# Kernel optimization log

Hardware: AMD Instinct MI355X
Metric: run time of the kernel (lower is better)

Reference implementation:

```python
import jax, jax.numpy as jnp
import numpy as np

NEG_INF = -9.0e15  # matches torch's -9000000000000000.0 mask value
ALPHA = 0.2        # LeakyReLU negative slope from init_kwargs


def setup_inputs() -> dict:
    key = jax.random.key(0)
    k1, k2, k3, k4, k5 = jax.random.split(key, 5)
    B, N, D, A = 64, 128, 128, 1000
    hidden = jax.random.normal(k1, (B, N, D), dtype=jnp.float32)
    adj = jax.random.randint(k2, (B, N, N), 0, 5)  # edge types 0..4 (0 = masked)
    a = jax.random.normal(k3, (D, 4), dtype=jnp.float32) * 0.1  # stacked a_0..a_3
    A_attr_sess = jax.random.uniform(k4, (B, N, A), dtype=jnp.float32)
    attr_embedding = jax.random.normal(k5, (A, D), dtype=jnp.float32)
    return {"hidden": hidden, "adj": adj, "a": a,
            "A_attr_sess": A_attr_sess, "attr_embedding": attr_embedding}


def reference(hidden, adj, a, A_attr_sess, attr_embedding):
    # a_input[b,i,j,:] = leaky_relu(h[b,i,:] * h[b,j,:])  -> [B,N,N,D]
    a_input = jax.nn.leaky_relu(hidden[:, :, None, :] * hidden[:, None, :, :],
                                negative_slope=ALPHA)
    # four edge-type scores in one contraction: [B,N,N,4]
    e = jnp.einsum('bijd,dk->bijk', a_input, a)
    # masked selection by adjacency edge type (later writes override earlier)
    alpha = jnp.full(adj.shape, NEG_INF, dtype=e.dtype)
    alpha = jnp.where(adj == 1, e[..., 0], alpha)
    alpha = jnp.where(adj == 2, e[..., 1], alpha)
    alpha = jnp.where(adj == 3, e[..., 2], alpha)
    alpha = jnp.where(adj == 4, e[..., 3], alpha)
    attn = jax.nn.softmax(alpha, axis=-1)        # [B,N,N]
    output = jnp.einsum('bij,bjd->bid', attn, hidden)  # [B,N,D]
    attr_sess = jnp.einsum('bna,ad->bnd', A_attr_sess, attr_embedding)
    return output, attr_sess
```

## Files before the change

### kernel.cpp

```cpp
#include <hip/hip_runtime.h>

#define BB 64
#define NN 128
#define DD 128
#define AA 1000
#define KPAD 1024
#define NEG_INF (-9.0e15f)

typedef __attribute__((ext_vector_type(8))) short short8;
typedef __attribute__((ext_vector_type(4))) float floatx4;
typedef __attribute__((ext_vector_type(4))) unsigned int uintx4;
typedef __attribute__((ext_vector_type(2))) unsigned int uintx2;

__device__ __forceinline__ float bflo(unsigned int u) { return __uint_as_float(u << 16); }
__device__ __forceinline__ float bfhi(unsigned int u) { return __uint_as_float(u & 0xffff0000u); }
__device__ __forceinline__ unsigned int packbf(float f0, float f1) {
  return (__float_as_uint(f0) >> 16) | (__float_as_uint(f1) & 0xffff0000u);
}
__device__ __forceinline__ unsigned short bf_rne(float f) {
  unsigned int u = __float_as_uint(f);
  return (unsigned short)((u + 0x7fffu + ((u >> 16) & 1u)) >> 16);
}
__device__ __forceinline__ unsigned int packbf_rne(float f0, float f1) {
  return (unsigned int)bf_rne(f0) | ((unsigned int)bf_rne(f1) << 16);
}
__device__ __forceinline__ short8 u2s(uintx4 v) {
  union { uintx4 u; short8 s; } x; x.u = v; return x.s;
}

__global__ __launch_bounds__(256) void prep_kernel(
    const float* __restrict__ hidden, const float* __restrict__ emb,
    unsigned short* __restrict__ ET, unsigned short* __restrict__ Hbf,
    unsigned short* __restrict__ HTg)
{
  const int t = threadIdx.x;
  const int bid = blockIdx.x;
  if (bid < BB) {
    __shared__ float hsf[NN * 129];
    const float* hb = hidden + (size_t)bid * NN * DD;
    #pragma unroll
    for (int u = 0; u < 16; ++u) {
      int e = u * 1024 + t * 4;
      float4 v = *reinterpret_cast<const float4*>(hb + e);
      int r = e >> 7, c = e & 127;
      float* d = &hsf[r * 129 + c];
      d[0] = v.x; d[1] = v.y; d[2] = v.z; d[3] = v.w;
    }
    __syncthreads();
    unsigned short* hb16 = Hbf + (size_t)bid * NN * DD;
    unsigned short* ht16 = HTg + (size_t)bid * NN * DD;
    #pragma unroll
    for (int u = 0; u < 8; ++u) {
      int e = u * 2048 + t * 8;
      int r = e >> 7, c = e & 127;
      const float* src = &hsf[r * 129 + c];
      uintx4 o;
      o.x = packbf_rne(src[0], src[1]); o.y = packbf_rne(src[2], src[3]);
      o.z = packbf_rne(src[4], src[5]); o.w = packbf_rne(src[6], src[7]);
      *reinterpret_cast<uintx4*>(hb16 + e) = o;
    }
    #pragma unroll
    for (int u = 0; u < 8; ++u) {
      int e = u * 2048 + t * 8;
      int dI = e >> 7, il = e & 127;
      float x[8];
      #pragma unroll
      for (int j = 0; j < 8; ++j) x[j] = hsf[(il + j) * 129 + dI];
      uintx4 o;
      o.x = packbf_rne(x[0], x[1]); o.y = packbf_rne(x[2], x[3]);
      o.z = packbf_rne(x[4], x[5]); o.w = packbf_rne(x[6], x[7]);
      *reinterpret_cast<uintx4*>(ht16 + e) = o;
    }
  } else {
    int c = bid - BB;
    int k0 = t * 4;
    float x[4];
    #pragma unroll
    for (int j = 0; j < 4; ++j) {
      int k = k0 + j;
      x[j] = (k < AA) ? emb[(size_t)k * DD + c] : 0.f;
    }
    uintx2 o;
    o.x = packbf_rne(x[0], x[1]);
    o.y = packbf_rne(x[2], x[3]);
    *reinterpret_cast<uintx2*>(ET + (size_t)c * KPAD + k0) = o;
  }
}

struct AttnSmem {
  __align__(16) unsigned short Hs[NN * 128];
  __align__(16) unsigned short As[4 * 16 * 256];
  __align__(16) float Sa[16 * 129];
  union {
    __align__(16) float saf[4 * 256];
    __align__(16) unsigned short W[16 * 128];
  } u;
};

__global__ __launch_bounds__(256, 2) void attn_kernel(
    const int* __restrict__ adj, const float* __restrict__ amat,
    const unsigned short* __restrict__ Hbf,
    const unsigned short* __restrict__ HTg,
    float* __restrict__ out0)
{
  __shared__ AttnSmem s;
  const int t = threadIdx.x;
  const int L = t & 63, w = t >> 6;
  const int lr = L & 15, lq = L >> 4;
  const int b = blockIdx.x >> 3;
  const int i0 = (blockIdx.x & 7) * 16;

  const unsigned short* hb = Hbf + (size_t)b * NN * DD;
  #pragma unroll
  for (int u = 0; u < 8; ++u) {
    int id = u * 256 + t;
    int r = id >> 4, c = id & 15;
    uintx4 v = *reinterpret_cast<const uintx4*>(hb + r * 128 + c * 8);
    *reinterpret_cast<uintx4*>(&s.Hs[r * 128 + ((c ^ (r & 15)) << 3)]) = v;
  }
  {
    float v1 = amat[t], v2 = amat[t + 256];
    int dI = t >> 2, k = t & 3;
    s.u.saf[k * 256 + dI] = 0.6f * v1;
    s.u.saf[k * 256 + 128 + dI] = 0.4f * v1;
    s.u.saf[k * 256 + 64 + dI] = 0.6f * v2;
    s.u.saf[k * 256 + 192 + dI] = 0.4f * v2;
  }
  __syncthreads();

  #pragma unroll
  for (int u = 0; u < 8; ++u) {
    int id = u * 256 + t;
    int k = id >> 9, ii = (id >> 5) & 15, c = id & 31;
    int srow = i0 + ii;
    int dchunk = c & 15;
    uintx4 hv = *reinterpret_cast<const uintx4*>(
        &s.Hs[srow * 128 + ((dchunk ^ (srow & 15)) << 3)]);
    if (c & 16) {
      hv.x &= 0x7fff7fffu; hv.y &= 0x7fff7fffu;
      hv.z &= 0x7fff7fffu; hv.w &= 0x7fff7fffu;
    }
    const float* sf = &s.u.saf[k * 256 + c * 8];
    uintx4 o;
    o.x = packbf(bflo(hv.x) * sf[0], bfhi(hv.x) * sf[1]);
    o.y = packbf(bflo(hv.y) * sf[2], bfhi(hv.y) * sf[3]);
    o.z = packbf(bflo(hv.z) * sf[4], bfhi(hv.z) * sf[5]);
    o.w = packbf(bflo(hv.w) * sf[6], bfhi(hv.w) * sf[7]);
    *reinterpret_cast<uintx4*>(&s.As[k * 4096 + ii * 256 + ((c ^ ii) << 3)]) = o;
  }
  __syncthreads();

  floatx4 acc[4][2];
  #pragma unroll
  for (int k = 0; k < 4; ++k)
    #pragma unroll
    for (int nt = 0; nt < 2; ++nt) acc[k][nt] = floatx4{0.f, 0.f, 0.f, 0.f};

  #pragma unroll
  for (int kt = 0; kt < 8; ++kt) {
    int ca = lq + 4 * kt;
    short8 afr[4];
    #pragma unroll
    for (int k = 0; k < 4; ++k)
      afr[k] = *reinterpret_cast<const short8*>(
          &s.As[k * 4096 + lr * 256 + ((ca ^ lr) << 3)]);
    int cb = lq + 4 * (kt & 3);
    short8 bfr[2];
    #pragma unroll
    for (int nt = 0; nt < 2; ++nt) {
      int jrow = w * 32 + nt * 16 + lr;
      uintx4 hv = *reinterpret_cast<const uintx4*>(
          &s.Hs[jrow * 128 + ((cb ^ (jrow & 15)) << 3)]);
      if (kt >= 4) {
        hv.x &= 0x7fff7fffu; hv.y &= 0x7fff7fffu;
        hv.z &= 0x7fff7fffu; hv.w &= 0x7fff7fffu;
      }
      bfr[nt] = u2s(hv);
    }
    #pragma unroll
    for (int k = 0; k < 4; ++k)
      #pragma unroll
      for (int nt = 0; nt < 2; ++nt)
        acc[k][nt] = __builtin_amdgcn_mfma_f32_16x16x32_bf16(
            afr[k], bfr[nt], acc[k][nt], 0, 0, 0);
  }

  short8 pvb[2][4];
  const unsigned short* ht = HTg + (size_t)b * NN * DD;
  #pragma unroll
  for (int nt = 0; nt < 2; ++nt)
    #pragma unroll
    for (int kt = 0; kt < 4; ++kt) {
      int dI = w * 32 + nt * 16 + lr;
      pvb[nt][kt] = *reinterpret_cast<const short8*>(ht + dI * 128 + kt * 32 + lq * 8);
    }

  const int* adjb = adj + ((size_t)b * NN + i0) * NN;
  #pragma unroll
  for (int nt = 0; nt < 2; ++nt)
    #pragma unroll
    for (int r = 0; r < 4; ++r) {
      int ii = lq * 4 + r;
      int j = w * 32 + nt * 16 + lr;
      int ad = adjb[ii * NN + j];
      float al = NEG_INF;
      al = (ad == 1) ? acc[0][nt][r] : al;
      al = (ad == 2) ? acc[1][nt][r] : al;
      al = (ad == 3) ? acc[2][nt][r] : al;
      al = (ad == 4) ? acc[3][nt][r] : al;
      s.Sa[ii * 129 + j] = al;
    }
  __syncthreads();

  #pragma unroll
  for (int p = 0; p < 4; ++p) {
    int ii = w * 4 + p;
    float a1 = s.Sa[ii * 129 + L];
    float a2 = s.Sa[ii * 129 + 64 + L];
    float m = fmaxf(a1, a2);
    #pragma unroll
    for (int off = 32; off > 0; off >>= 1) m = fmaxf(m, __shfl_xor(m, off, 64));
    float e1 = __expf(fmaxf(a1 - m, -80.f));
    float e2 = __expf(fmaxf(a2 - m, -80.f));
    float ss = e1 + e2;
    #pragma unroll
    for (int off = 32; off > 0; off >>= 1) ss += __shfl_xor(ss, off, 64);
    float inv = 1.f / ss;
    int j2 = L + 64;
    s.u.W[ii * 128 + (((L >> 3) ^ ii) << 3) + (L & 7)] = bf_rne(e1 * inv);
    s.u.W[ii * 128 + (((j2 >> 3) ^ ii) << 3) + (j2 & 7)] = bf_rne(e2 * inv);
  }
  __syncthreads();

  floatx4 oacc[2];
  oacc[0] = floatx4{0.f, 0.f, 0.f, 0.f};
  oacc[1] = floatx4{0.f, 0.f, 0.f, 0.f};
  #pragma unroll
  for (int kt = 0; kt < 4; ++kt) {
    int c = lq + 4 * kt;
    short8 wf = *reinterpret_cast<const short8*>(
        &s.u.W[lr * 128 + ((c ^ lr) << 3)]);
    #pragma unroll
    for (int nt = 0; nt < 2; ++nt)
      oacc[nt] = __builtin_amdgcn_mfma_f32_16x16x32_bf16(
          wf, pvb[nt][kt], oacc[nt], 0, 0, 0);
  }
  float* ob = out0 + ((size_t)b * NN + i0) * DD;
  #pragma unroll
  for (int nt = 0; nt < 2; ++nt)
    #pragma unroll
    for (int r = 0; r < 4; ++r)
      ob[(lq * 4 + r) * DD + w * 32 + nt * 16 + lr] = oacc[nt][r];
}

#define BK 64
__global__ __launch_bounds__(256) void attr_kernel(
    const float* __restrict__ Aattr, const unsigned short* __restrict__ ET,
    float* __restrict__ out1)
{
  __shared__ __align__(16) unsigned short ETs[2][DD * BK];
  __shared__ __align__(16) unsigned short As2[2][32 * BK];

  const int t = threadIdx.x;
  const int L = t & 63, w = t >> 6;
  const int lr = L & 15, lq = L >> 4;
  const int r0 = blockIdx.x * 32;

  float4 pa0, pa1;
  uintx4 pe[4];
  const int ar = t >> 3, ak = (t & 7) * 8;
  const int ec = t >> 1, ej0 = (t & 1) * 4;

  auto fetch = [&](int it) {
    int kb = it * BK;
    int k4 = kb + ak;
    float4 z = {0.f, 0.f, 0.f, 0.f};
    pa0 = (k4 < AA) ? *reinterpret_cast<const float4*>(Aattr + (size_t)(r0 + ar) * AA + k4) : z;
    pa1 = (k4 + 4 < AA) ? *reinterpret_cast<const float4*>(Aattr + (size_t)(r0 + ar) * AA + k4 + 4) : z;
    #pragma unroll
    for (int q = 0; q < 4; ++q)
      pe[q] = *reinterpret_cast<const uintx4*>(ET + (size_t)ec * KPAD + kb + (ej0 + q) * 8);
  };
  auto stage = [&](int buf) {
    uintx4 o;
    o.x = packbf(pa0.x, pa0.y); o.y = packbf(pa0.z, pa0.w);
    o.z = packbf(pa1.x, pa1.y); o.w = packbf(pa1.z, pa1.w);
    int ac = t & 7;
    *reinterpret_cast<uintx4*>(&As2[buf][ar * BK + ((ac ^ (ar & 7)) << 3)]) = o;
    #pragma unroll
    for (int q = 0; q < 4; ++q)
      *reinterpret_cast<uintx4*>(&ETs[buf][ec * BK + (((ej0 + q) ^ (ec & 7)) << 3)]) = pe[q];
  };

  floatx4 acc[2][2];
  #pragma unroll
  for (int mt = 0; mt < 2; ++mt)
    #pragma unroll
    for (int nt = 0; nt < 2; ++nt) acc[mt][nt] = floatx4{0.f, 0.f, 0.f, 0.f};

  fetch(0);
  for (int it = 0; it < 16; ++it) {
    stage(it & 1);
    __syncthreads();
    if (it < 15) fetch(it + 1);
    #pragma unroll
    for (int ks = 0; ks < 2; ++ks) {
      int c = lq + 4 * ks;
      short8 af[2], bf[2];
      #pragma unroll
      for (int mt = 0; mt < 2; ++mt) {
        int row = mt * 16 + lr;
        af[mt] = *reinterpret_cast<const short8*>(
            &As2[it & 1][row * BK + ((c ^ (row & 7)) << 3)]);
      }
      #pragma unroll
      for (int nt = 0; nt < 2; ++nt) {
        int n = w * 32 + nt * 16 + lr;
        bf[nt] = *reinterpret_cast<const short8*>(
            &ETs[it & 1][n * BK + ((c ^ (n & 7)) << 3)]);
      }
      #pragma unroll
      for (int mt = 0; mt < 2; ++mt)
        #pragma unroll
        for (int nt = 0; nt < 2; ++nt)
          acc[mt][nt] = __builtin_amdgcn_mfma_f32_16x16x32_bf16(
              af[mt], bf[nt], acc[mt][nt], 0, 0, 0);
    }
  }

  float* ob = out1 + (size_t)r0 * DD;
  #pragma unroll
  for (int mt = 0; mt < 2; ++mt)
    #pragma unroll
    for (int nt = 0; nt < 2; ++nt)
      #pragma unroll
      for (int r = 0; r < 4; ++r)
        ob[(mt * 16 + lq * 4 + r) * DD + w * 32 + nt * 16 + lr] = acc[mt][nt][r];
}

extern "C" void kernel_launch(void* const* d_in, const int* in_sizes, int n_in,
                              void* d_out, int out_size, void* d_ws, size_t ws_size,
                              hipStream_t stream) {
  const float* hidden = (const float*)d_in[0];
  const int*   adj    = (const int*)d_in[1];
  const float* amat   = (const float*)d_in[2];
  const float* Aattr  = (const float*)d_in[3];
  const float* emb    = (const float*)d_in[4];

  float* out0 = (float*)d_out;
  float* out1 = out0 + (size_t)BB * NN * DD;

  unsigned short* ET  = (unsigned short*)d_ws;
  unsigned short* Hbf = ET + (size_t)DD * KPAD;
  unsigned short* HTg = Hbf + (size_t)BB * NN * DD;

  prep_kernel<<<BB + DD, 256, 0, stream>>>(hidden, emb, ET, Hbf, HTg);
  attn_kernel<<<BB * 8, 256, 0, stream>>>(adj, amat, Hbf, HTg, out0);
  attr_kernel<<<(BB * NN) / 32, 256, 0, stream>>>(Aattr, ET, out1);
}
```

Before: 109.8 us.

## Fuse attention and attribute GEMM into one launch with shared-memory union

Merges the attention and attribute-projection kernels into a single 768-block launch that branches on block index, so the two independent workloads run concurrently and one launch is saved. The attention path now reads fp32 hidden directly and converts to bf16 on load, dropping the bf16 copy of hidden that the prep kernel used to write. Adjacency is loaded up front so its latency overlaps the MFMA work. Shared memory is reorganised as a union to reduce the footprint, and occupancy is raised to 3 blocks per CU. The cost is an extra barrier, larger fp32 loads per attention block, and mixed block types that may balance unevenly across CUs.

```diff
diff --git a/kernel.cpp b/kernel.cpp
--- a/kernel.cpp
+++ b/kernel.cpp
@@ -30,8 +30,7 @@
 
 __global__ __launch_bounds__(256) void prep_kernel(
     const float* __restrict__ hidden, const float* __restrict__ emb,
-    unsigned short* __restrict__ ET, unsigned short* __restrict__ Hbf,
-    unsigned short* __restrict__ HTg)
+    unsigned short* __restrict__ ET, unsigned short* __restrict__ HTg)
 {
   const int t = threadIdx.x;
   const int bid = blockIdx.x;
@@ -47,18 +46,7 @@
       d[0] = v.x; d[1] = v.y; d[2] = v.z; d[3] = v.w;
     }
     __syncthreads();
-    unsigned short* hb16 = Hbf + (size_t)bid * NN * DD;
     unsigned short* ht16 = HTg + (size_t)bid * NN * DD;
-    #pragma unroll
-    for (int u = 0; u < 8; ++u) {
-      int e = u * 2048 + t * 8;
-      int r = e >> 7, c = e & 127;
-      const float* src = &hsf[r * 129 + c];
-      uintx4 o;
-      o.x = packbf_rne(src[0], src[1]); o.y = packbf_rne(src[2], src[3]);
-      o.z = packbf_rne(src[4], src[5]); o.w = packbf_rne(src[6], src[7]);
-      *reinterpret_cast<uintx4*>(hb16 + e) = o;
-    }
     #pragma unroll
     for (int u = 0; u < 8; ++u) {
       int e = u * 2048 + t * 8;
@@ -89,42 +77,63 @@
 
 struct AttnSmem {
   __align__(16) unsigned short Hs[NN * 128];
-  __align__(16) unsigned short As[4 * 16 * 256];
-  __align__(16) float Sa[16 * 129];
   union {
-    __align__(16) float saf[4 * 256];
-    __align__(16) unsigned short W[16 * 128];
-  } u;
+    __align__(16) unsigned short As[4 * 16 * 256];
+    struct {
+      __align__(16) float Sa[16 * 129];
+      __align__(16) unsigned short W[16 * 128];
+    } sw;
+  } u2;
+  __align__(16) float saf[4 * 256];
 };
 
-__global__ __launch_bounds__(256, 2) void attn_kernel(
+#define BK 64
+struct AttrSmem {
+  __align__(16) unsigned short ETs[2][DD * BK];
+  __align__(16) unsigned short As2[2][32 * BK];
+};
+
+union FusedSmem { AttnSmem a; AttrSmem g; };
+
+__device__ __forceinline__ void attn_body(
+    AttnSmem& s, const float* __restrict__ hidden,
     const int* __restrict__ adj, const float* __restrict__ amat,
-    const unsigned short* __restrict__ Hbf,
-    const unsigned short* __restrict__ HTg,
-    float* __restrict__ out0)
+    const unsigned short* __restrict__ HTg, float* __restrict__ out0)
 {
-  __shared__ AttnSmem s;
   const int t = threadIdx.x;
   const int L = t & 63, w = t >> 6;
   const int lr = L & 15, lq = L >> 4;
   const int b = blockIdx.x >> 3;
   const int i0 = (blockIdx.x & 7) * 16;
 
-  const unsigned short* hb = Hbf + (size_t)b * NN * DD;
+  const int* adjb = adj + ((size_t)b * NN + i0) * NN;
+  int adjv[8];
+  #pragma unroll
+  for (int nt = 0; nt < 2; ++nt)
+    #pragma unroll
+    for (int r = 0; r < 4; ++r)
+      adjv[nt * 4 + r] = adjb[(lq * 4 + r) * NN + w * 32 + nt * 16 + lr];
+
+  const float* hb = hidden + (size_t)b * NN * DD;
   #pragma unroll
   for (int u = 0; u < 8; ++u) {
     int id = u * 256 + t;
     int r = id >> 4, c = id & 15;
-    uintx4 v = *reinterpret_cast<const uintx4*>(hb + r * 128 + c * 8);
-    *reinterpret_cast<uintx4*>(&s.Hs[r * 128 + ((c ^ (r & 15)) << 3)]) = v;
+    const float* src = hb + r * 128 + c * 8;
+    float4 v0 = *reinterpret_cast<const float4*>(src);
+    float4 v1 = *reinterpret_cast<const float4*>(src + 4);
+    uintx4 o;
+    o.x = packbf_rne(v0.x, v0.y); o.y = packbf_rne(v0.z, v0.w);
+    o.z = packbf_rne(v1.x, v1.y); o.w = packbf_rne(v1.z, v1.w);
+    *reinterpret_cast<uintx4*>(&s.Hs[r * 128 + ((c ^ (r & 15)) << 3)]) = o;
   }
   {
     float v1 = amat[t], v2 = amat[t + 256];
     int dI = t >> 2, k = t & 3;
-    s.u.saf[k * 256 + dI] = 0.6f * v1;
-    s.u.saf[k * 256 + 128 + dI] = 0.4f * v1;
-    s.u.saf[k * 256 + 64 + dI] = 0.6f * v2;
-    s.u.saf[k * 256 + 192 + dI] = 0.4f * v2;
+    s.saf[k * 256 + dI] = 0.6f * v1;
+    s.saf[k * 256 + 128 + dI] = 0.4f * v1;
+    s.saf[k * 256 + 64 + dI] = 0.6f * v2;
+    s.saf[k * 256 + 192 + dI] = 0.4f * v2;
   }
   __syncthreads();
 
@@ -140,13 +149,13 @@
       hv.x &= 0x7fff7fffu; hv.y &= 0x7fff7fffu;
       hv.z &= 0x7fff7fffu; hv.w &= 0x7fff7fffu;
     }
-    const float* sf = &s.u.saf[k * 256 + c * 8];
+    const float* sf = &s.saf[k * 256 + c * 8];
     uintx4 o;
     o.x = packbf(bflo(hv.x) * sf[0], bfhi(hv.x) * sf[1]);
     o.y = packbf(bflo(hv.y) * sf[2], bfhi(hv.y) * sf[3]);
     o.z = packbf(bflo(hv.z) * sf[4], bfhi(hv.z) * sf[5]);
     o.w = packbf(bflo(hv.w) * sf[6], bfhi(hv.w) * sf[7]);
-    *reinterpret_cast<uintx4*>(&s.As[k * 4096 + ii * 256 + ((c ^ ii) << 3)]) = o;
+    *reinterpret_cast<uintx4*>(&s.u2.As[k * 4096 + ii * 256 + ((c ^ ii) << 3)]) = o;
   }
   __syncthreads();
 
@@ -163,7 +172,7 @@
     #pragma unroll
     for (int k = 0; k < 4; ++k)
       afr[k] = *reinterpret_cast<const short8*>(
-          &s.As[k * 4096 + lr * 256 + ((ca ^ lr) << 3)]);
+          &s.u2.As[k * 4096 + lr * 256 + ((ca ^ lr) << 3)]);
     int cb = lq + 4 * (kt & 3);
     short8 bfr[2];
     #pragma unroll
@@ -184,6 +193,7 @@
         acc[k][nt] = __builtin_amdgcn_mfma_f32_16x16x32_bf16(
             afr[k], bfr[nt], acc[k][nt], 0, 0, 0);
   }
+  __syncthreads();
 
   short8 pvb[2][4];
   const unsigned short* ht = HTg + (size_t)b * NN * DD;
@@ -195,28 +205,27 @@
       pvb[nt][kt] = *reinterpret_cast<const short8*>(ht + dI * 128 + kt * 32 + lq * 8);
     }
 
-  const int* adjb = adj + ((size_t)b * NN + i0) * NN;
   #pragma unroll
   for (int nt = 0; nt < 2; ++nt)
     #pragma unroll
     for (int r = 0; r < 4; ++r) {
       int ii = lq * 4 + r;
       int j = w * 32 + nt * 16 + lr;
-      int ad = adjb[ii * NN + j];
+      int ad = adjv[nt * 4 + r];
       float al = NEG_INF;
       al = (ad == 1) ? acc[0][nt][r] : al;
       al = (ad == 2) ? acc[1][nt][r] : al;
       al = (ad == 3) ? acc[2][nt][r] : al;
       al = (ad == 4) ? acc[3][nt][r] : al;
-      s.Sa[ii * 129 + j] = al;
+      s.u2.sw.Sa[ii * 129 + j] = al;
     }
   __syncthreads();
 
   #pragma unroll
   for (int p = 0; p < 4; ++p) {
     int ii = w * 4 + p;
-    float a1 = s.Sa[ii * 129 + L];
-    float a2 = s.Sa[ii * 129 + 64 + L];
+    float a1 = s.u2.sw.Sa[ii * 129 + L];
+    float a2 = s.u2.sw.Sa[ii * 129 + 64 + L];
     float m = fmaxf(a1, a2);
     #pragma unroll
     for (int off = 32; off > 0; off >>= 1) m = fmaxf(m, __shfl_xor(m, off, 64));
@@ -227,8 +236,8 @@
     for (int off = 32; off > 0; off >>= 1) ss += __shfl_xor(ss, off, 64);
     float inv = 1.f / ss;
     int j2 = L + 64;
-    s.u.W[ii * 128 + (((L >> 3) ^ ii) << 3) + (L & 7)] = bf_rne(e1 * inv);
-    s.u.W[ii * 128 + (((j2 >> 3) ^ ii) << 3) + (j2 & 7)] = bf_rne(e2 * inv);
+    s.u2.sw.W[ii * 128 + (((L >> 3) ^ ii) << 3) + (L & 7)] = bf_rne(e1 * inv);
+    s.u2.sw.W[ii * 128 + (((j2 >> 3) ^ ii) << 3) + (j2 & 7)] = bf_rne(e2 * inv);
   }
   __syncthreads();
 
@@ -239,7 +248,7 @@
   for (int kt = 0; kt < 4; ++kt) {
     int c = lq + 4 * kt;
     short8 wf = *reinterpret_cast<const short8*>(
-        &s.u.W[lr * 128 + ((c ^ lr) << 3)]);
+        &s.u2.sw.W[lr * 128 + ((c ^ lr) << 3)]);
     #pragma unroll
     for (int nt = 0; nt < 2; ++nt)
       oacc[nt] = __builtin_amdgcn_mfma_f32_16x16x32_bf16(
@@ -253,18 +262,14 @@
       ob[(lq * 4 + r) * DD + w * 32 + nt * 16 + lr] = oacc[nt][r];
 }
 
-#define BK 64
-__global__ __launch_bounds__(256) void attr_kernel(
-    const float* __restrict__ Aattr, const unsigned short* __restrict__ ET,
-    float* __restrict__ out1)
+__device__ __forceinline__ void attr_body(
+    AttrSmem& s, const float* __restrict__ Aattr,
+    const unsigned short* __restrict__ ET, float* __restrict__ out1)
 {
-  __shared__ __align__(16) unsigned short ETs[2][DD * BK];
-  __shared__ __align__(16) unsigned short As2[2][32 * BK];
-
   const int t = threadIdx.x;
   const int L = t & 63, w = t >> 6;
   const int lr = L & 15, lq = L >> 4;
-  const int r0 = blockIdx.x * 32;
+  const int r0 = (blockIdx.x - 512) * 32;
 
   float4 pa0, pa1;
   uintx4 pe[4];
@@ -286,10 +291,10 @@
     o.x = packbf(pa0.x, pa0.y); o.y = packbf(pa0.z, pa0.w);
     o.z = packbf(pa1.x, pa1.y); o.w = packbf(pa1.z, pa1.w);
     int ac = t & 7;
-    *reinterpret_cast<uintx4*>(&As2[buf][ar * BK + ((ac ^ (ar & 7)) << 3)]) = o;
+    *reinterpret_cast<uintx4*>(&s.As2[buf][ar * BK + ((ac ^ (ar & 7)) << 3)]) = o;
     #pragma unroll
     for (int q = 0; q < 4; ++q)
-      *reinterpret_cast<uintx4*>(&ETs[buf][ec * BK + (((ej0 + q) ^ (ec & 7)) << 3)]) = pe[q];
+      *reinterpret_cast<uintx4*>(&s.ETs[buf][ec * BK + (((ej0 + q) ^ (ec & 7)) << 3)]) = pe[q];
   };
 
   floatx4 acc[2][2];
@@ -311,13 +316,13 @@
       for (int mt = 0; mt < 2; ++mt) {
         int row = mt * 16 + lr;
         af[mt] = *reinterpret_cast<const short8*>(
-            &As2[it & 1][row * BK + ((c ^ (row & 7)) << 3)]);
+            &s.As2[it & 1][row * BK + ((c ^ (row & 7)) << 3)]);
       }
       #pragma unroll
       for (int nt = 0; nt < 2; ++nt) {
         int n = w * 32 + nt * 16 + lr;
         bf[nt] = *reinterpret_cast<const short8*>(
-            &ETs[it & 1][n * BK + ((c ^ (n & 7)) << 3)]);
+            &s.ETs[it & 1][n * BK + ((c ^ (n & 7)) << 3)]);
       }
       #pragma unroll
       for (int mt = 0; mt < 2; ++mt)
@@ -336,6 +341,17 @@
       #pragma unroll
       for (int r = 0; r < 4; ++r)
         ob[(mt * 16 + lq * 4 + r) * DD + w * 32 + nt * 16 + lr] = acc[mt][nt][r];
+}
+
+__global__ __launch_bounds__(256, 3) void fused_kernel(
+    const float* __restrict__ hidden, const int* __restrict__ adj,
+    const float* __restrict__ amat, const float* __restrict__ Aattr,
+    const unsigned short* __restrict__ ET, const unsigned short* __restrict__ HTg,
+    float* __restrict__ out0, float* __restrict__ out1)
+{
+  __shared__ FusedSmem sm;
+  if (blockIdx.x < 512) attn_body(sm.a, hidden, adj, amat, HTg, out0);
+  else                  attr_body(sm.g, Aattr, ET, out1);
 }
 
 extern "C" void kernel_launch(void* const* d_in, const int* in_sizes, int n_in,
@@ -351,10 +367,9 @@
   float* out1 = out0 + (size_t)BB * NN * DD;
 
   unsigned short* ET  = (unsigned short*)d_ws;
-  unsigned short* Hbf = ET + (size_t)DD * KPAD;
-  unsigned short* HTg = Hbf + (size_t)BB * NN * DD;
-
-  prep_kernel<<<BB + DD, 256, 0, stream>>>(hidden, emb, ET, Hbf, HTg);
-  attn_kernel<<<BB * 8, 256, 0, stream>>>(adj, amat, Hbf, HTg, out0);
-  attr_kernel<<<(BB * NN) / 32, 256, 0, stream>>>(Aattr, ET, out1);
-}
+  unsigned short* HTg = ET + (size_t)DD * KPAD;
+
+  prep_kernel<<<BB + DD, 256, 0, stream>>>(hidden, emb, ET, HTg);
+  fused_kernel<<<768, 256, 0, stream>>>(hidden, adj, amat, Aattr, ET, HTg,
+                                        out0, out1);
+}
```

Measured after the change: 106.8 us, median of 2. 1.03x faster.
